# Kernel optimization log

Measured on AMD Instinct MI355X. Metric: run time of the kernel, lower is better.

Reference implementation:

```python
import jax, jax.numpy as jnp
import numpy as np
from jax import lax

SCALE = 2
KSIZE = 5
RGB_RANGE = 255.0
RGB_MEAN = (0.4488, 0.4371, 0.404)


def setup_inputs() -> dict:
    key = jax.random.key(0)
    ks = jax.random.split(key, 8)
    N, C, H, W = 4, 3, 128, 128
    G0 = 64
    s = SCALE
    x = jax.random.normal(ks[0], (N, C, H, W), dtype=jnp.float32)
    # relative position matrix: (1, (H*s)*(W*s), 3), values in [0,1)
    pos_mat = jax.random.uniform(ks[1], (1, H * s * W * s, 3), dtype=jnp.float32)
    conv_w = jax.random.normal(ks[2], (G0, C, KSIZE, KSIZE), dtype=jnp.float32) * 0.05
    conv_b = jax.random.normal(ks[3], (G0,), dtype=jnp.float32) * 0.05
    w1 = jax.random.normal(ks[4], (3, 256), dtype=jnp.float32) * 0.05
    b1 = jax.random.normal(ks[5], (256,), dtype=jnp.float32) * 0.05
    w2 = jax.random.normal(ks[6], (256, 9 * G0 * 3), dtype=jnp.float32) * 0.05
    b2 = jax.random.normal(ks[7], (9 * G0 * 3,), dtype=jnp.float32) * 0.05
    return {"x": x, "pos_mat": pos_mat, "conv_w": conv_w, "conv_b": conv_b,
            "w1": w1, "b1": b1, "w2": w2, "b2": b2}


def _unfold3(feat):
    # torch F.unfold(feat, 3, padding=1) ordering: channel-major then (ki, kj)
    N, C, H, W = feat.shape
    p = jnp.pad(feat, ((0, 0), (0, 0), (1, 1), (1, 1)))
    patches = jnp.stack([p[:, :, i:i + H, j:j + W]
                         for i in range(3) for j in range(3)], axis=2)  # [N,C,9,H,W]
    return patches.reshape(N, C * 9, H * W)  # [N, C*9, L]


def reference(x, pos_mat, conv_w, conv_b, w1, b1, w2, b2):
    s = SCALE
    N, _, H, W = x.shape
    # Feature extraction: conv5x5 (SAME) + ReLU
    feat = lax.conv_general_dilated(x, conv_w, (1, 1), 'SAME',
                                    dimension_numbers=('NCHW', 'OIHW', 'NCHW'))
    feat = jax.nn.relu(feat + conv_b[None, :, None, None])  # [N, G0, H, W]
    G0 = feat.shape[1]
    K = G0 * 9
    # Pos2Weight MLP: per output-pixel dynamic conv weights
    p = pos_mat.reshape(-1, 3)  # [(H*s)*(W*s), 3]
    lw = jax.nn.relu(p @ w1 + b1) @ w2 + b2  # [(H*s)*(W*s), K*3]
    # reshape to [s^2, H*W, K, 3] matching torch permute pipeline
    lw = lw.reshape(H, s, W, s, K, 3).transpose(1, 3, 0, 2, 4, 5).reshape(s * s, H * W, K, 3)
    # unfold 3x3 patches (repeat_x just tiles identical copies; compute once)
    cols = _unfold3(feat).transpose(0, 2, 1)  # [N, L, K], L = H*W
    # per-pixel matmul: out[n,p,l,c] = sum_k cols[n,l,k] * lw[p,l,k,c]
    out = jnp.einsum('nlk,plkc->nplc', cols, lw)  # [N, s^2, L, 3]
    # pixel-shuffle style rearrangement to [N, 3, H*s, W*s]
    out = out.reshape(N, s, s, H, W, 3).transpose(0, 5, 3, 1, 4, 2)
    out = out.reshape(N, 3, H * s, W * s)
    # add_mean (MeanShift sign=+1, std=1)
    mean = jnp.asarray(RGB_MEAN, dtype=out.dtype) * RGB_RANGE
    return out + mean[None, :, None, None]
```

## Files before the change

### kernel.cpp

```cpp
#include <hip/hip_runtime.h>

#define HW   128
#define OHW  256
#define G0n  64
#define HID  256
#define NOUT 1728
#define NB   4

typedef __attribute__((ext_vector_type(8))) short bf16x8;
typedef __attribute__((ext_vector_type(4))) float f32x4;
typedef __attribute__((ext_vector_type(4))) unsigned int u32x4;
typedef __attribute__((ext_vector_type(2))) unsigned int u32x2;

__device__ __forceinline__ unsigned short f2bf(float f) {
    unsigned int u = __builtin_bit_cast(unsigned int, f);
    u += 0x7fffu + ((u >> 16) & 1u);
    return (unsigned short)(u >> 16);
}
__device__ __forceinline__ float bflo(unsigned int d) {
    return __builtin_bit_cast(float, d << 16);
}
__device__ __forceinline__ float bfhi(unsigned int d) {
    return __builtin_bit_cast(float, d & 0xffff0000u);
}

__global__ __launch_bounds__(256) void prep_w2t(const float* __restrict__ w2,
                                                unsigned short* __restrict__ w2t) {
    __shared__ float t[64][65];
    int kb = blockIdx.x & 3, cb = blockIdx.x >> 2;
    int lc = threadIdx.x & 63, lr = threadIdx.x >> 6;
    #pragma unroll
    for (int i = 0; i < 16; ++i) {
        int kk = lr + i * 4;
        t[kk][lc] = w2[(kb * 64 + kk) * NOUT + cb * 64 + lc];
    }
    __syncthreads();
    #pragma unroll
    for (int i = 0; i < 16; ++i) {
        int cc = lr + i * 4;
        w2t[(cb * 64 + cc) * 256 + kb * 64 + lc] = f2bf(t[lc][cc]);
    }
}

__global__ __launch_bounds__(256) void conv5_relu_kernel(
    const float* __restrict__ x, const float* __restrict__ cw,
    const float* __restrict__ cb, float* __restrict__ feat)
{
    int idx = blockIdx.x * 256 + threadIdx.x;
    int w4 = (idx & 31) * 4;
    int h  = (idx >> 5) & 127;
    int g  = (idx >> 12) & 63;
    int n  = idx >> 18;
    float bv = cb[g];
    float a[4] = {bv, bv, bv, bv};
    const float* wp = cw + g * 75;
    #pragma unroll
    for (int ci = 0; ci < 3; ++ci) {
        const float* xr = x + (n * 3 + ci) * (HW * HW);
        #pragma unroll
        for (int ki = 0; ki < 5; ++ki) {
            int hh = h + ki - 2;
            if (hh < 0 || hh >= HW) continue;
            const float* row = xr + hh * HW;
            float f[8];
            if (w4 != 0 && w4 != 124) {
                float2 u0 = *(const float2*)(row + w4 - 2);
                float2 u1 = *(const float2*)(row + w4);
                float2 u2 = *(const float2*)(row + w4 + 2);
                float2 u3 = *(const float2*)(row + w4 + 4);
                f[0] = u0.x; f[1] = u0.y; f[2] = u1.x; f[3] = u1.y;
                f[4] = u2.x; f[5] = u2.y; f[6] = u3.x; f[7] = u3.y;
            } else {
                #pragma unroll
                for (int j = 0; j < 8; ++j) {
                    int ww = w4 - 2 + j;
                    f[j] = (ww >= 0 && ww < HW) ? row[ww] : 0.0f;
                }
            }
            float wt[5];
            #pragma unroll
            for (int kj = 0; kj < 5; ++kj) wt[kj] = wp[ci * 25 + ki * 5 + kj];
            #pragma unroll
            for (int j = 0; j < 4; ++j)
                #pragma unroll
                for (int kj = 0; kj < 5; ++kj)
                    a[j] = fmaf(f[j + kj], wt[kj], a[j]);
        }
    }
    float4 o;
    o.x = fmaxf(a[0], 0.f); o.y = fmaxf(a[1], 0.f);
    o.z = fmaxf(a[2], 0.f); o.w = fmaxf(a[3], 0.f);
    *(float4*)&feat[((n * G0n + g) * HW + h) * HW + w4] = o;
}

__global__ __launch_bounds__(256, 2) void fused_metasr_mfma(
    const float* __restrict__ feat, const unsigned short* __restrict__ w2t,
    const float* __restrict__ pos,  const float* __restrict__ w1,
    const float* __restrict__ b1,   const float* __restrict__ b2,
    float* __restrict__ out)
{
    __shared__ __align__(16) unsigned short AL[64 * 260];
    __shared__ __align__(16) unsigned short FT[64 * 6 * 4 * 8];

    const int tid = threadIdx.x;
    const int bx = blockIdx.x & 31, by = blockIdx.x >> 5;
    const int oy0 = by * 8, ox0 = bx * 8;
    const int h0 = by * 4,  w0 = bx * 4;

    for (int i = tid; i < 64 * 6 * 4 * 8; i += 256) {
        int c  = i & 7;
        int n  = (i >> 3) & 3;
        int r  = (i >> 5) % 6;
        int ci = (i >> 5) / 6;
        int gh = h0 - 1 + r, gw = w0 - 1 + c;
        float v = 0.0f;
        if (c < 6 && gh >= 0 && gh < HW && gw >= 0 && gw < HW)
            v = feat[((n * G0n + ci) * HW + gh) * HW + gw];
        FT[i] = f2bf(v);
    }

    {
        int px = tid >> 2, q = tid & 3;
        int rr = (oy0 + (px >> 3)) * OHW + (ox0 + (px & 7));
        float p0 = pos[rr * 3 + 0], p1 = pos[rr * 3 + 1], p2 = pos[rr * 3 + 2];
        #pragma unroll
        for (int j = 0; j < 16; ++j) {
            int k0 = q * 4 + j * 16;
            float4 wa = *(const float4*)&w1[k0];
            float4 wb = *(const float4*)&w1[HID + k0];
            float4 wc = *(const float4*)&w1[2 * HID + k0];
            float4 bb = *(const float4*)&b1[k0];
            unsigned short h0s = f2bf(fmaxf(fmaf(p0, wa.x, fmaf(p1, wb.x, fmaf(p2, wc.x, bb.x))), 0.f));
            unsigned short h1s = f2bf(fmaxf(fmaf(p0, wa.y, fmaf(p1, wb.y, fmaf(p2, wc.y, bb.y))), 0.f));
            unsigned short h2s = f2bf(fmaxf(fmaf(p0, wa.z, fmaf(p1, wb.z, fmaf(p2, wc.z, bb.z))), 0.f));
            unsigned short h3s = f2bf(fmaxf(fmaf(p0, wa.w, fmaf(p1, wb.w, fmaf(p2, wc.w, bb.w))), 0.f));
            u32x2 pk;
            pk.x = (unsigned)h0s | ((unsigned)h1s << 16);
            pk.y = (unsigned)h2s | ((unsigned)h3s << 16);
            *(u32x2*)&AL[px * 260 + k0] = pk;
        }
    }
    __syncthreads();

    const int lane = tid & 63, nq = tid >> 6;
    const int cl = lane & 15, hi = lane >> 4;
    bf16x8 afrag[4][8];
    #pragma unroll
    for (int m = 0; m < 4; ++m)
        #pragma unroll
        for (int k8 = 0; k8 < 8; ++k8)
            afrag[m][k8] = *(const bf16x8*)&AL[(m * 16 + cl) * 260 + k8 * 32 + hi * 8];

    const int epx = tid >> 2, en = tid & 3;
    const int iy = (epx >> 3) >> 1;
    const int ix = (epx & 7) >> 1;
    const bool selhi = (ix >= 2);
    const bool podd  = (ix & 1) != 0;
    const unsigned lwbase = (unsigned)(epx * 520);
    float oacc0 = 0.f, oacc1 = 0.f, oacc2 = 0.f;

    for (int ch = 0; ch < 9; ++ch) {
        f32x4 acc[4][3];
        #pragma unroll
        for (int m = 0; m < 4; ++m)
            #pragma unroll
            for (int j = 0; j < 3; ++j)
                acc[m][j] = (f32x4){0.f, 0.f, 0.f, 0.f};

        #pragma unroll
        for (int kh = 0; kh < 2; ++kh) {
            #pragma unroll
            for (int kk = 0; kk < 4; ++kk) {
                bf16x8 bfrag[3];
                #pragma unroll
                for (int j = 0; j < 3; ++j) {
                    int col = nq * 48 + j * 16 + cl;
                    bfrag[j] = *(const bf16x8*)&w2t[(ch * 192 + col) * 256 + kh * 128 + kk * 32 + hi * 8];
                }
                #pragma unroll
                for (int m = 0; m < 4; ++m)
                    #pragma unroll
                    for (int j = 0; j < 3; ++j)
                        acc[m][j] = __builtin_amdgcn_mfma_f32_16x16x32_bf16(
                            afrag[m][kh * 4 + kk], bfrag[j], acc[m][j], 0, 0, 0);
            }
        }

        __syncthreads();
        #pragma unroll
        for (int j = 0; j < 3; ++j) {
            int col = nq * 48 + j * 16 + cl;
            float bv = b2[ch * 192 + col];
            int kt = col / 3;
            int c  = col - kt * 3;
            #pragma unroll
            for (int m = 0; m < 4; ++m)
                #pragma unroll
                for (int r = 0; r < 4; ++r) {
                    int row = m * 16 + hi * 4 + r;
                    AL[row * 260 + kt * 4 + c] = f2bf(acc[m][j][r] + bv);
                }
        }
        __syncthreads();

        int k0 = ch * 64;
        int t3a = k0 / 3;
        int t3b = (k0 + 63) / 3;
        auto do_t3 = [&](int t3, bool guard) {
            int ci = t3 / 3;
            int di = t3 - ci * 3;
            const char* fp = (const char*)FT + ci * 384 + (iy + di) * 64 + en * 16;
            u32x4 w = *(const u32x4*)fp;
            unsigned a0 = selhi ? w.y : w.x;
            unsigned b0 = selhi ? w.z : w.y;
            float loa = bflo(a0), hia = bfhi(a0);
            float lob = bflo(b0), hib = bfhi(b0);
            float f0 = podd ? hia : loa;
            float f1 = podd ? lob : hia;
            float f2 = podd ? hib : lob;
            int ktb = 3 * t3 - k0;
            #pragma unroll
            for (int dj = 0; dj < 3; ++dj) {
                int kt = ktb + dj;
                float fv = dj == 0 ? f0 : (dj == 1 ? f1 : f2);
                if (guard) {
                    fv = ((unsigned)kt < 64u) ? fv : 0.0f;
                    kt = kt < 0 ? 0 : (kt > 63 ? 63 : kt);
                }
                u32x2 d = *(const u32x2*)((const char*)AL + lwbase + (unsigned)(kt * 8));
                oacc0 = fmaf(fv, bflo(d.x), oacc0);
                oacc1 = fmaf(fv, bfhi(d.x), oacc1);
                oacc2 = fmaf(fv, bflo(d.y), oacc2);
            }
        };
        do_t3(t3a, true);
        for (int t3 = t3a + 1; t3 < t3b; ++t3) do_t3(t3, false);
        do_t3(t3b, true);
    }

    int oy = oy0 + (epx >> 3), ox = ox0 + (epx & 7);
    out[((en * 3 + 0) * OHW + oy) * OHW + ox] = oacc0 + 0.4488f * 255.0f;
    out[((en * 3 + 1) * OHW + oy) * OHW + ox] = oacc1 + 0.4371f * 255.0f;
    out[((en * 3 + 2) * OHW + oy) * OHW + ox] = oacc2 + 0.4040f * 255.0f;
}

extern "C" void kernel_launch(void* const* d_in, const int* in_sizes, int n_in,
                              void* d_out, int out_size, void* d_ws, size_t ws_size,
                              hipStream_t stream) {
    (void)in_sizes; (void)n_in; (void)out_size; (void)ws_size;
    const float* x      = (const float*)d_in[0];
    const float* posm   = (const float*)d_in[1];
    const float* conv_w = (const float*)d_in[2];
    const float* conv_b = (const float*)d_in[3];
    const float* w1     = (const float*)d_in[4];
    const float* b1     = (const float*)d_in[5];
    const float* w2     = (const float*)d_in[6];
    const float* b2     = (const float*)d_in[7];
    float* out = (float*)d_out;

    unsigned short* w2t = (unsigned short*)d_ws;
    float* feat = (float*)((char*)d_ws + 884736);

    prep_w2t<<<108, 256, 0, stream>>>(w2, w2t);
    conv5_relu_kernel<<<(NB * G0n * HW * 32) / 256, 256, 0, stream>>>(x, conv_w, conv_b, feat);
    fused_metasr_mfma<<<1024, 256, 0, stream>>>(feat, w2t, posm, w1, b1, b2, out);
}
```

Measured before the change: 235.1 us.

## Split fused MetaSR kernel into GEMM-to-global and separate einsum kernel

Splits the fused kernel in two. The first kernel computes the Pos2Weight local weights with MFMA and writes them to a global bf16 workspace (about 226 MB). The second kernel reloads those weights per pixel from global memory into registers and does the per-pixel einsum against a bf16 feature tile held in LDS. This removes the per-chunk LDS reshuffle and the barriers between the GEMM and the reduction, but adds a large round trip through HBM and a second launch.

Result: slower. 240.4 us (+2.3%).

```diff
diff --git a/kernel.cpp b/kernel.cpp
--- a/kernel.cpp
+++ b/kernel.cpp
@@ -93,31 +93,16 @@
     *(float4*)&feat[((n * G0n + g) * HW + h) * HW + w4] = o;
 }
 
-__global__ __launch_bounds__(256, 2) void fused_metasr_mfma(
-    const float* __restrict__ feat, const unsigned short* __restrict__ w2t,
-    const float* __restrict__ pos,  const float* __restrict__ w1,
-    const float* __restrict__ b1,   const float* __restrict__ b2,
-    float* __restrict__ out)
+__global__ __launch_bounds__(256) void gemm_lw(
+    const unsigned short* __restrict__ w2t, const float* __restrict__ pos,
+    const float* __restrict__ w1, const float* __restrict__ b1,
+    const float* __restrict__ b2, unsigned short* __restrict__ lw)
 {
     __shared__ __align__(16) unsigned short AL[64 * 260];
-    __shared__ __align__(16) unsigned short FT[64 * 6 * 4 * 8];
 
     const int tid = threadIdx.x;
     const int bx = blockIdx.x & 31, by = blockIdx.x >> 5;
     const int oy0 = by * 8, ox0 = bx * 8;
-    const int h0 = by * 4,  w0 = bx * 4;
-
-    for (int i = tid; i < 64 * 6 * 4 * 8; i += 256) {
-        int c  = i & 7;
-        int n  = (i >> 3) & 3;
-        int r  = (i >> 5) % 6;
-        int ci = (i >> 5) / 6;
-        int gh = h0 - 1 + r, gw = w0 - 1 + c;
-        float v = 0.0f;
-        if (c < 6 && gh >= 0 && gh < HW && gw >= 0 && gw < HW)
-            v = feat[((n * G0n + ci) * HW + gh) * HW + gw];
-        FT[i] = f2bf(v);
-    }
 
     {
         int px = tid >> 2, q = tid & 3;
@@ -150,14 +135,10 @@
         #pragma unroll
         for (int k8 = 0; k8 < 8; ++k8)
             afrag[m][k8] = *(const bf16x8*)&AL[(m * 16 + cl) * 260 + k8 * 32 + hi * 8];
-
-    const int epx = tid >> 2, en = tid & 3;
-    const int iy = (epx >> 3) >> 1;
-    const int ix = (epx & 7) >> 1;
-    const bool selhi = (ix >= 2);
-    const bool podd  = (ix & 1) != 0;
-    const unsigned lwbase = (unsigned)(epx * 520);
-    float oacc0 = 0.f, oacc1 = 0.f, oacc2 = 0.f;
+    __syncthreads();
+
+    const size_t rowbase = (size_t)blockIdx.x * 64;
+    const int srow = tid >> 2, sq = tid & 3;
 
     for (int ch = 0; ch < 9; ++ch) {
         f32x4 acc[4][3];
@@ -166,82 +147,118 @@
             #pragma unroll
             for (int j = 0; j < 3; ++j)
                 acc[m][j] = (f32x4){0.f, 0.f, 0.f, 0.f};
-
-        #pragma unroll
-        for (int kh = 0; kh < 2; ++kh) {
-            #pragma unroll
-            for (int kk = 0; kk < 4; ++kk) {
-                bf16x8 bfrag[3];
-                #pragma unroll
-                for (int j = 0; j < 3; ++j) {
-                    int col = nq * 48 + j * 16 + cl;
-                    bfrag[j] = *(const bf16x8*)&w2t[(ch * 192 + col) * 256 + kh * 128 + kk * 32 + hi * 8];
+        #pragma unroll
+        for (int ks = 0; ks < 8; ++ks) {
+            bf16x8 bfrag[3];
+            #pragma unroll
+            for (int j = 0; j < 3; ++j) {
+                int col = ch * 192 + nq * 48 + j * 16 + cl;
+                bfrag[j] = *(const bf16x8*)&w2t[(size_t)col * 256 + ks * 32 + hi * 8];
+            }
+            #pragma unroll
+            for (int m = 0; m < 4; ++m)
+                #pragma unroll
+                for (int j = 0; j < 3; ++j)
+                    acc[m][j] = __builtin_amdgcn_mfma_f32_16x16x32_bf16(
+                        afrag[m][ks], bfrag[j], acc[m][j], 0, 0, 0);
+        }
+        #pragma unroll
+        for (int j = 0; j < 3; ++j) {
+            int lcol = nq * 48 + j * 16 + cl;
+            float bv = b2[ch * 192 + lcol];
+            #pragma unroll
+            for (int m = 0; m < 4; ++m)
+                #pragma unroll
+                for (int r = 0; r < 4; ++r)
+                    AL[(m * 16 + hi * 4 + r) * 200 + lcol] = f2bf(acc[m][j][r] + bv);
+        }
+        __syncthreads();
+        unsigned short* dst = lw + (rowbase + srow) * NOUT + ch * 192;
+        #pragma unroll
+        for (int s = 0; s < 6; ++s) {
+            int off = (sq + s * 4) * 8;
+            *(u32x4*)(dst + off) = *(const u32x4*)&AL[srow * 200 + off];
+        }
+        __syncthreads();
+    }
+}
+
+__global__ __launch_bounds__(256) void einsum_out(
+    const float* __restrict__ feat, const unsigned short* __restrict__ lw,
+    float* __restrict__ out)
+{
+    __shared__ __align__(8) unsigned short FT[64 * 6 * 4 * 6];
+
+    const int tid = threadIdx.x;
+    const int bx = blockIdx.x & 31, by = blockIdx.x >> 5;
+    const int oy0 = by * 8, ox0 = bx * 8;
+    const int h0 = by * 4,  w0 = bx * 4;
+
+    for (int i = tid; i < 64 * 6 * 4 * 6; i += 256) {
+        int c = i % 6;
+        int t = i / 6;
+        int n = t & 3;
+        t >>= 2;
+        int r  = t % 6;
+        int ci = t / 6;
+        int gh = h0 - 1 + r, gw = w0 - 1 + c;
+        float v = 0.0f;
+        if (gh >= 0 && gh < HW && gw >= 0 && gw < HW)
+            v = feat[((n * G0n + ci) * HW + gh) * HW + gw];
+        FT[i] = f2bf(v);
+    }
+    __syncthreads();
+
+    const int px = tid >> 2, n = tid & 3;
+    const int iy = (px >> 3) >> 1;
+    const int ix = (px & 7) >> 1;
+    const bool podd = (ix & 1) != 0;
+    const int ixa = ix & ~1;
+
+    const u32x4* lwp = (const u32x4*)(lw + ((size_t)blockIdx.x * 64 + px) * NOUT);
+    float o0 = 0.f, o1 = 0.f, o2 = 0.f;
+
+    for (int g = 0; g < 8; ++g) {
+        u32x4 LA[14], LB[14];
+        #pragma unroll
+        for (int t = 0; t < 14; ++t) LA[t] = lwp[g * 27 + t];
+        #pragma unroll
+        for (int t = 0; t < 14; ++t) LB[t] = (t + 13 < 27) ? lwp[g * 27 + 13 + t] : (u32x4){0,0,0,0};
+
+        #pragma unroll
+        for (int cl8 = 0; cl8 < 8; ++cl8) {
+            int ci = g * 8 + cl8;
+            float fv[9];
+            #pragma unroll
+            for (int di = 0; di < 3; ++di) {
+                int rb = ((ci * 6 + iy + di) * 4 + n) * 6 + ixa;
+                unsigned u0 = *(const unsigned*)&FT[rb];
+                unsigned u1 = *(const unsigned*)&FT[rb + 2];
+                fv[di * 3 + 0] = podd ? bfhi(u0) : bflo(u0);
+                fv[di * 3 + 1] = podd ? bflo(u1) : bfhi(u0);
+                fv[di * 3 + 2] = podd ? bfhi(u1) : bflo(u1);
+            }
+            #pragma unroll
+            for (int ktl = 0; ktl < 9; ++ktl) {
+                #pragma unroll
+                for (int c = 0; c < 3; ++c) {
+                    int idx = cl8 * 27 + ktl * 3 + c;
+                    unsigned d;
+                    if (idx < 108) d = LA[idx >> 3][(idx >> 1) & 3];
+                    else { int i2 = idx - 104; d = LB[i2 >> 3][(i2 >> 1) & 3]; }
+                    float v = (idx & 1) ? bfhi(d) : bflo(d);
+                    if (c == 0) o0 = fmaf(fv[ktl], v, o0);
+                    else if (c == 1) o1 = fmaf(fv[ktl], v, o1);
+                    else o2 = fmaf(fv[ktl], v, o2);
                 }
-                #pragma unroll
-                for (int m = 0; m < 4; ++m)
-                    #pragma unroll
-                    for (int j = 0; j < 3; ++j)
-                        acc[m][j] = __builtin_amdgcn_mfma_f32_16x16x32_bf16(
-                            afrag[m][kh * 4 + kk], bfrag[j], acc[m][j], 0, 0, 0);
-            }
-        }
-
-        __syncthreads();
-        #pragma unroll
-        for (int j = 0; j < 3; ++j) {
-            int col = nq * 48 + j * 16 + cl;
-            float bv = b2[ch * 192 + col];
-            int kt = col / 3;
-            int c  = col - kt * 3;
-            #pragma unroll
-            for (int m = 0; m < 4; ++m)
-                #pragma unroll
-                for (int r = 0; r < 4; ++r) {
-                    int row = m * 16 + hi * 4 + r;
-                    AL[row * 260 + kt * 4 + c] = f2bf(acc[m][j][r] + bv);
-                }
-        }
-        __syncthreads();
-
-        int k0 = ch * 64;
-        int t3a = k0 / 3;
-        int t3b = (k0 + 63) / 3;
-        auto do_t3 = [&](int t3, bool guard) {
-            int ci = t3 / 3;
-            int di = t3 - ci * 3;
-            const char* fp = (const char*)FT + ci * 384 + (iy + di) * 64 + en * 16;
-            u32x4 w = *(const u32x4*)fp;
-            unsigned a0 = selhi ? w.y : w.x;
-            unsigned b0 = selhi ? w.z : w.y;
-            float loa = bflo(a0), hia = bfhi(a0);
-            float lob = bflo(b0), hib = bfhi(b0);
-            float f0 = podd ? hia : loa;
-            float f1 = podd ? lob : hia;
-            float f2 = podd ? hib : lob;
-            int ktb = 3 * t3 - k0;
-            #pragma unroll
-            for (int dj = 0; dj < 3; ++dj) {
-                int kt = ktb + dj;
-                float fv = dj == 0 ? f0 : (dj == 1 ? f1 : f2);
-                if (guard) {
-                    fv = ((unsigned)kt < 64u) ? fv : 0.0f;
-                    kt = kt < 0 ? 0 : (kt > 63 ? 63 : kt);
-                }
-                u32x2 d = *(const u32x2*)((const char*)AL + lwbase + (unsigned)(kt * 8));
-                oacc0 = fmaf(fv, bflo(d.x), oacc0);
-                oacc1 = fmaf(fv, bfhi(d.x), oacc1);
-                oacc2 = fmaf(fv, bflo(d.y), oacc2);
-            }
-        };
-        do_t3(t3a, true);
-        for (int t3 = t3a + 1; t3 < t3b; ++t3) do_t3(t3, false);
-        do_t3(t3b, true);
-    }
-
-    int oy = oy0 + (epx >> 3), ox = ox0 + (epx & 7);
-    out[((en * 3 + 0) * OHW + oy) * OHW + ox] = oacc0 + 0.4488f * 255.0f;
-    out[((en * 3 + 1) * OHW + oy) * OHW + ox] = oacc1 + 0.4371f * 255.0f;
-    out[((en * 3 + 2) * OHW + oy) * OHW + ox] = oacc2 + 0.4040f * 255.0f;
+            }
+        }
+    }
+
+    int oy = oy0 + (px >> 3), ox = ox0 + (px & 7);
+    out[((n * 3 + 0) * OHW + oy) * OHW + ox] = o0 + 0.4488f * 255.0f;
+    out[((n * 3 + 1) * OHW + oy) * OHW + ox] = o1 + 0.4371f * 255.0f;
+    out[((n * 3 + 2) * OHW + oy) * OHW + ox] = o2 + 0.4040f * 255.0f;
 }
 
 extern "C" void kernel_launch(void* const* d_in, const int* in_sizes, int n_in,
@@ -260,8 +277,11 @@
 
     unsigned short* w2t = (unsigned short*)d_ws;
     float* feat = (float*)((char*)d_ws + 884736);
+    const size_t lw_off = 884736u + 16777216u;
+    unsigned short* lwbuf = (unsigned short*)((char*)d_ws + lw_off);
 
     prep_w2t<<<108, 256, 0, stream>>>(w2, w2t);
     conv5_relu_kernel<<<(NB * G0n * HW * 32) / 256, 256, 0, stream>>>(x, conv_w, conv_b, feat);
-    fused_metasr_mfma<<<1024, 256, 0, stream>>>(feat, w2t, posm, w1, b1, b2, out);
-}
+    gemm_lw<<<1024, 256, 0, stream>>>(w2t, posm, w1, b1, b2, lwbuf);
+    einsum_out<<<1024, 256, 0, stream>>>(feat, lwbuf, out);
+}
```
